# Kernel optimization log

Measured on AMD Instinct MI355X. Metric: run time of the kernel, lower is better.

## Reference

```python
import itertools
import jax, jax.numpy as jnp
import numpy as np
from jax import lax

INT_STEPS = 7
DOWN = 2


def _sample(vol, coords):
    """Trilinear sample vol [C, D, H, W] at voxel coords [3, D2, H2, W2].
    Matches torch grid_sample(align_corners=True, padding_mode='zeros') after
    voxelmorph's voxel->[-1,1] normalization (i.e. plain voxel coordinates)."""
    dims = vol.shape[1:]
    c0f = jnp.floor(coords)
    frac = coords - c0f
    c0 = c0f.astype(jnp.int32)
    out = jnp.zeros((vol.shape[0],) + coords.shape[1:], vol.dtype)
    for corner in itertools.product((0, 1), repeat=3):
        w = jnp.ones(coords.shape[1:], vol.dtype)
        valid = True
        idxs = []
        for ax in range(3):
            idx = c0[ax] + corner[ax]
            w = w * (frac[ax] if corner[ax] else 1.0 - frac[ax])
            valid = valid & (idx >= 0) & (idx < dims[ax])
            idxs.append(jnp.clip(idx, 0, dims[ax] - 1))
        out = out + vol[:, idxs[0], idxs[1], idxs[2]] * (w * valid)
    return out


def _grid(shape, dtype):
    return jnp.stack(jnp.meshgrid(*[jnp.arange(s, dtype=dtype) for s in shape], indexing='ij'))


def _warp(src, flow):
    # SpatialTransformer: sample src at identity grid + flow (voxel coords)
    return _sample(src, _grid(src.shape[1:], flow.dtype) + flow)


def _resize(x, out_shape):
    # F.interpolate trilinear, align_corners=True: src = i*(in-1)/(out-1)
    coords = jnp.stack(jnp.meshgrid(
        *[jnp.linspace(0.0, s_in - 1.0, s_out, dtype=x.dtype)
          for s_in, s_out in zip(x.shape[1:], out_shape)], indexing='ij'))
    return _sample(x, coords)


def _flow_single(pos_flow, label):
    # pos_flow: [3, D, H, W], label: [1, D, H, W]
    full = pos_flow.shape[1:]
    down_shape = tuple(s // DOWN for s in full)
    # ResizeTransform(int_downsize): factor=1/DOWN<1 -> resize then scale
    f = _resize(pos_flow, down_shape) * (1.0 / DOWN)
    # VecInt: scaling and squaring
    f = f * (1.0 / (2 ** INT_STEPS))
    for _ in range(INT_STEPS):
        f = f + _warp(f, f)
    # ResizeTransform(1/int_downsize): factor=DOWN>1 -> scale then resize
    f = _resize(f * float(DOWN), full)
    moved = _warp(label, f)
    return moved, f


def setup_inputs() -> dict:
    key = jax.random.key(0)
    k1, k2, k3 = jax.random.split(key, 3)
    B, F, D, H, W = 1, 16, 128, 128, 128
    features = jax.random.normal(k1, (B, F, D, H, W), jnp.float32)
    moving_label = jax.random.uniform(k2, (B, 1, D, H, W), jnp.float32)
    # conv weight initialized Normal(0, 1e-5), bias zeros (as in module)
    weight = jax.random.normal(k3, (3, F, 3, 3, 3), jnp.float32) * 1e-5
    bias = jnp.zeros((3,), jnp.float32)
    return {"features": features, "moving_label": moving_label,
            "weight": weight, "bias": bias}


def reference(features, moving_label, weight, bias):
    pos_flow = lax.conv_general_dilated(
        features, weight, window_strides=(1, 1, 1),
        padding=[(1, 1)] * 3,
        dimension_numbers=('NCDHW', 'OIDHW', 'NCDHW'))
    pos_flow = pos_flow + bias[None, :, None, None, None]
    moved, flow = jax.vmap(_flow_single)(pos_flow, moving_label)
    return moved, flow
```

## Files before the change

### kernel.cpp

```cpp
#include <hip/hip_runtime.h>


#define V128 2097152
#define V64  262144

typedef __attribute__((ext_vector_type(2))) float f32x2;
typedef float f32x2u __attribute__((ext_vector_type(2), aligned(4)));

template <int C>
__device__ __forceinline__ void trisample(const float* __restrict__ vol,
                                          int D, int H, int W, int cstride,
                                          float cz, float cy, float cx,
                                          float* out) {
    float fz = floorf(cz), fy = floorf(cy), fx = floorf(cx);
    int iz = (int)fz, iy = (int)fy, ix = (int)fx;
    float tz = cz - fz, ty = cy - fy, tx = cx - fx;
#pragma unroll
    for (int c = 0; c < C; ++c) out[c] = 0.0f;
#pragma unroll
    for (int dz = 0; dz < 2; ++dz) {
#pragma unroll
        for (int dy = 0; dy < 2; ++dy) {
#pragma unroll
            for (int dx = 0; dx < 2; ++dx) {
                int z = iz + dz, y = iy + dy, x = ix + dx;
                float w = (dz ? tz : 1.0f - tz) *
                          (dy ? ty : 1.0f - ty) *
                          (dx ? tx : 1.0f - tx);
                bool valid = (z >= 0) && (z < D) && (y >= 0) && (y < H) &&
                             (x >= 0) && (x < W);
                int zc = min(max(z, 0), D - 1);
                int yc = min(max(y, 0), H - 1);
                int xc = min(max(x, 0), W - 1);
                int base = (zc * H + yc) * W + xc;
                float wv = valid ? w : 0.0f;
#pragma unroll
                for (int c = 0; c < C; ++c)
                    out[c] += vol[c * cstride + base] * wv;
            }
        }
    }
}

template <int SI>
__device__ __forceinline__ void lds_lerp3(const float* __restrict__ f,
                                          float pz, float py, float px,
                                          float* out) {
    constexpr int NI = SI * SI * SI;
    float fz = floorf(pz), fy = floorf(py), fx = floorf(px);
    int iz = (int)fz, iy = (int)fy, ix = (int)fx;
    float tz = pz - fz, ty = py - fy, tx = px - fx;
    int b = (iz * SI + iy) * SI + ix;
    float wz0 = 1.0f - tz, wy0 = 1.0f - ty, wx0 = 1.0f - tx;
#pragma unroll
    for (int c = 0; c < 3; ++c) {
        const float* fc = f + c * NI;
        float v00 = fc[b] * wx0 + fc[b + 1] * tx;
        float v01 = fc[b + SI] * wx0 + fc[b + SI + 1] * tx;
        float v10 = fc[b + SI * SI] * wx0 + fc[b + SI * SI + 1] * tx;
        float v11 = fc[b + SI * SI + SI] * wx0 + fc[b + SI * SI + SI + 1] * tx;
        out[c] = wz0 * (wy0 * v00 + ty * v01) + tz * (wy0 * v10 + ty * v11);
    }
}

template <int SI, int NT>
__device__ __forceinline__ void step_lds(const float* __restrict__ in,
                                         float* __restrict__ out, int tid) {
    constexpr int SO = SI - 2;
    constexpr int NI = SI * SI * SI;
    constexpr int NO = SO * SO * SO;
    for (int i = tid; i < NO; i += NT) {
        int xx = i % SO, yy = (i / SO) % SO, zz = i / (SO * SO);
        int la = ((zz + 1) * SI + (yy + 1)) * SI + (xx + 1);
        float fz = in[la], fy = in[la + NI], fx = in[la + 2 * NI];
        float sm[3];
        lds_lerp3<SI>(in, (zz + 1) + fz, (yy + 1) + fy, (xx + 1) + fx, sm);
        out[i] = fz + sm[0];
        out[i + NO] = fy + sm[1];
        out[i + 2 * NO] = fx + sm[2];
    }
}

template <int NT>
__device__ __forceinline__ void step_to_global(const float* __restrict__ in,
                                               float* __restrict__ gout,
                                               int tx, int ty, int tz,
                                               int tid) {
    constexpr int SI = 10;
    constexpr int NI = SI * SI * SI;
    for (int i = tid; i < 512; i += NT) {
        int xx = i & 7, yy = (i >> 3) & 7, zz = i >> 6;
        int la = ((zz + 1) * SI + (yy + 1)) * SI + (xx + 1);
        float fz = in[la], fy = in[la + NI], fx = in[la + 2 * NI];
        float sm[3];
        lds_lerp3<SI>(in, (zz + 1) + fz, (yy + 1) + fy, (xx + 1) + fx, sm);
        int n3 = ((((tz + zz) << 12) + ((ty + yy) << 6) + (tx + xx))) * 3;
        gout[n3] = fz + sm[0];
        gout[n3 + 1] = fy + sm[1];
        gout[n3 + 2] = fx + sm[2];
    }
}

__global__ __launch_bounds__(256) void conv_kernel(
    const float* __restrict__ feat, const float* __restrict__ weight,
    const float* __restrict__ bias, float* __restrict__ pf) {
    __shared__ float smem[2][4356];
    const int tid = threadIdx.x;
    const int x0 = blockIdx.x * 64, y0 = blockIdx.y * 4, z0 = blockIdx.z * 8;
    const int lx = tid & 63, ly = tid >> 6;

    int goff[16];
    int laddr[16];
    unsigned vmask = 0;
#pragma unroll
    for (int k = 0; k < 16; ++k) {
        int s = tid + 256 * k;
        int col = s / 10;
        int zz = s - col * 10;
        int xx = col % 66;
        int yy = col / 66;
        laddr[k] = col * 11 + zz;
        bool intile = (k < 15) || (tid < 120);
        int gx = x0 + xx - 1, gy = y0 + yy - 1, gz = z0 + zz - 1;
        bool ok = intile && ((unsigned)gx < 128u) && ((unsigned)gy < 128u) &&
                  ((unsigned)gz < 128u);
        goff[k] = (gz << 14) + (gy << 7) + gx;
        if (ok) vmask |= (1u << k);
    }

    f32x2 acc[3][4];
#pragma unroll
    for (int o = 0; o < 3; ++o)
#pragma unroll
        for (int zp = 0; zp < 4; ++zp) acc[o][zp] = (f32x2)(0.0f);

    {
        float vals[16];
#pragma unroll
        for (int k = 0; k < 16; ++k) {
            vals[k] = 0.0f;
            if (vmask & (1u << k)) vals[k] = feat[goff[k]];
        }
#pragma unroll
        for (int k = 0; k < 16; ++k)
            if (k < 15 || tid < 120) smem[0][laddr[k]] = vals[k];
    }

    for (int c = 0; c < 16; ++c) {
        __syncthreads();
        if (c + 1 < 16) {
            const float* fc = feat + ((c + 1) << 21);
            float* buf = smem[(c + 1) & 1];
            float vals[16];
#pragma unroll
            for (int k = 0; k < 16; ++k) {
                vals[k] = 0.0f;
                if (vmask & (1u << k)) vals[k] = fc[goff[k]];
            }
#pragma unroll
            for (int k = 0; k < 16; ++k)
                if (k < 15 || tid < 120) buf[laddr[k]] = vals[k];
        }
        const float* buf = smem[c & 1];
        const float* wc = weight + c * 27;
#pragma unroll
        for (int dy = 0; dy < 3; ++dy) {
#pragma unroll
            for (int dx = 0; dx < 3; ++dx) {
                const float* p = buf + ((ly + dy) * 66 + lx + dx) * 11;
                f32x2 pv[5];
                f32x2 qv[4];
#pragma unroll
                for (int k2 = 0; k2 < 5; ++k2)
                    pv[k2] = *(const f32x2u*)(p + 2 * k2);
#pragma unroll
                for (int k2 = 0; k2 < 4; ++k2)
                    qv[k2] = *(const f32x2u*)(p + 2 * k2 + 1);
#pragma unroll
                for (int o = 0; o < 3; ++o) {
                    float w0 = wc[o * 432 + 0 + dy * 3 + dx];
                    float w1 = wc[o * 432 + 9 + dy * 3 + dx];
                    float w2 = wc[o * 432 + 18 + dy * 3 + dx];
#pragma unroll
                    for (int zp = 0; zp < 4; ++zp) {
                        acc[o][zp] += pv[zp] * (f32x2)(w0);
                        acc[o][zp] += qv[zp] * (f32x2)(w1);
                        acc[o][zp] += pv[zp + 1] * (f32x2)(w2);
                    }
                }
            }
        }
    }

    float b0 = bias[0], b1 = bias[1], b2 = bias[2];
#pragma unroll
    for (int zp = 0; zp < 4; ++zp) {
        int vox0 = ((z0 + 2 * zp) << 14) + ((y0 + ly) << 7) + x0 + lx;
#pragma unroll
        for (int h = 0; h < 2; ++h) {
            int m3 = (vox0 + (h << 14)) * 3;
            pf[m3] = (h ? acc[0][zp].y : acc[0][zp].x) + b0;
            pf[m3 + 1] = (h ? acc[1][zp].y : acc[1][zp].x) + b1;
            pf[m3 + 2] = (h ? acc[2][zp].y : acc[2][zp].x) + b2;
        }
    }
}

__global__ __launch_bounds__(512) void f2_kernel(
    const float* __restrict__ pf, float* __restrict__ gout) {
    __shared__ float A[3 * 2744];
    __shared__ float B[3 * 1728];
    const int tid = threadIdx.x;
    const int tx = blockIdx.x * 8, ty = blockIdx.y * 8, tz = blockIdx.z * 8;
    const int rbx = tx - 3, rby = ty - 3, rbz = tz - 3;
    const float s2 = 127.0f / 63.0f;
    const float k = 1.0f / 256.0f;
    for (int i = tid; i < 2744; i += 512) {
        int xx = i % 14, yy = (i / 14) % 14, zz = i / 196;
        int gz = rbz + zz, gy = rby + yy, gx = rbx + xx;
        float v0 = 0.0f, v1 = 0.0f, v2 = 0.0f;
        if ((unsigned)gz < 64u && (unsigned)gy < 64u && (unsigned)gx < 64u) {
            float cz = gz * s2, cy = gy * s2, cx = gx * s2;
            int iz = min((int)cz, 126);
            int iy = min((int)cy, 126);
            int ix = min((int)cx, 126);
            float tzf = cz - (float)iz;
            float tyf = cy - (float)iy;
            float txf = cx - (float)ix;
            float wz[2] = {1.0f - tzf, tzf};
            float wy[2] = {1.0f - tyf, tyf};
            float wx[2] = {1.0f - txf, txf};
            int b = ((iz << 14) + (iy << 7) + ix) * 3;
#pragma unroll
            for (int dz = 0; dz < 2; ++dz)
#pragma unroll
                for (int dy = 0; dy < 2; ++dy)
#pragma unroll
                    for (int dx = 0; dx < 2; ++dx) {
                        float w = wz[dz] * wy[dy] * wx[dx];
                        int bb = b + dz * (3 << 14) + dy * (3 << 7) + dx * 3;
                        v0 += pf[bb] * w;
                        v1 += pf[bb + 1] * w;
                        v2 += pf[bb + 2] * w;
                    }
        }
        A[i] = v0 * k;
        A[i + 2744] = v1 * k;
        A[i + 2 * 2744] = v2 * k;
    }
    __syncthreads();
    step_lds<14, 512>(A, B, tid);
    __syncthreads();
    step_lds<12, 512>(B, A, tid);
    __syncthreads();
    step_to_global<512>(A, gout, tx, ty, tz, tid);
}

__global__ __launch_bounds__(512) void f3_kernel(
    const float* __restrict__ gin, float* __restrict__ gout) {
    __shared__ float A[3 * 2744];
    __shared__ float B[3 * 1728];
    const int tid = threadIdx.x;
    const int tx = blockIdx.x * 8, ty = blockIdx.y * 8, tz = blockIdx.z * 8;
    const int rbx = tx - 3, rby = ty - 3, rbz = tz - 3;
    for (int i = tid; i < 2744; i += 512) {
        int xx = i % 14, yy = (i / 14) % 14, zz = i / 196;
        int gz = rbz + zz, gy = rby + yy, gx = rbx + xx;
        float v0 = 0.0f, v1 = 0.0f, v2 = 0.0f;
        if ((unsigned)gz < 64u && (unsigned)gy < 64u && (unsigned)gx < 64u) {
            int n3 = ((gz << 12) + (gy << 6) + gx) * 3;
            v0 = gin[n3];
            v1 = gin[n3 + 1];
            v2 = gin[n3 + 2];
        }
        A[i] = v0;
        A[i + 2744] = v1;
        A[i + 2 * 2744] = v2;
    }
    __syncthreads();
    step_lds<14, 512>(A, B, tid);
    __syncthreads();
    step_lds<12, 512>(B, A, tid);
    __syncthreads();
    step_to_global<512>(A, gout, tx, ty, tz, tid);
}

__global__ __launch_bounds__(512) void f4_kernel(
    const float* __restrict__ gin, const float* __restrict__ label,
    float* __restrict__ moved, float* __restrict__ flow) {
    __shared__ float A[3 * 2197];
    __shared__ float B[3 * 1331];
    const int tid = threadIdx.x;
    const int ttx = blockIdx.x, tty = blockIdx.y, ttz = blockIdx.z;
    const int r0x = (1008 * ttx) / 127 - 1;
    const int r0y = (1008 * tty) / 127 - 1;
    const int r0z = (1008 * ttz) / 127 - 1;
    const int rbx = r0x - 1, rby = r0y - 1, rbz = r0z - 1;
    for (int i = tid; i < 2197; i += 512) {
        int xx = i % 13, yy = (i / 13) % 13, zz = i / 169;
        int gz = rbz + zz, gy = rby + yy, gx = rbx + xx;
        float v0 = 0.0f, v1 = 0.0f, v2 = 0.0f;
        if ((unsigned)gz < 64u && (unsigned)gy < 64u && (unsigned)gx < 64u) {
            int n3 = ((gz << 12) + (gy << 6) + gx) * 3;
            v0 = gin[n3];
            v1 = gin[n3 + 1];
            v2 = gin[n3 + 2];
        }
        A[i] = v0;
        A[i + 2197] = v1;
        A[i + 2 * 2197] = v2;
    }
    __syncthreads();
    step_lds<13, 512>(A, B, tid);
    __syncthreads();
    const float s3 = 63.0f / 127.0f;
    for (int i = tid; i < 4096; i += 512) {
        int lx = i & 15, ly = (i >> 4) & 15, lz = i >> 8;
        int gx = ttx * 16 + lx, gy = tty * 16 + ly, gz = ttz * 16 + lz;
        float f[3];
        lds_lerp3<11>(B, gz * s3 - (float)r0z, gy * s3 - (float)r0y,
                      gx * s3 - (float)r0x, f);
        float fz = 2.0f * f[0], fy = 2.0f * f[1], fx = 2.0f * f[2];
        int m = (gz << 14) + (gy << 7) + gx;
        flow[m] = fz;
        flow[m + V128] = fy;
        flow[m + 2 * V128] = fx;
        float mv[1];
        trisample<1>(label, 128, 128, 128, 0, gz + fz, gy + fy, gx + fx, mv);
        moved[m] = mv[0];
    }
}

extern "C" void kernel_launch(void* const* d_in, const int* in_sizes, int n_in,
                              void* d_out, int out_size, void* d_ws,
                              size_t ws_size, hipStream_t stream) {
    const float* features = (const float*)d_in[0];
    const float* label = (const float*)d_in[1];
    const float* weight = (const float*)d_in[2];
    const float* bias = (const float*)d_in[3];
    float* out = (float*)d_out;
    float* moved = out;
    float* flow = out + V128;
    float* fA = (float*)d_ws;
    float* fB = fA + 3 * V64;

    conv_kernel<<<dim3(2, 32, 16), 256, 0, stream>>>(features, weight, bias,
                                                     flow);
    f2_kernel<<<dim3(8, 8, 8), 512, 0, stream>>>(flow, fA);
    f3_kernel<<<dim3(8, 8, 8), 512, 0, stream>>>(fA, fB);
    f4_kernel<<<dim3(8, 8, 8), 512, 0, stream>>>(fB, label, moved, flow);
}
```

Before: 325.3 us.

## Split downsample into separate kernel and reorder conv LDS load mapping

The downsample resize moves out of the first squaring kernel into a standalone per-voxel kernel that writes to the unused 'moved' output buffer. Both squaring stages then reuse one generic f23 kernel. Before, each block resampled its whole halo region, so overlapping halos were downsampled repeatedly; now every voxel is downsampled once. The cost is an extra launch and a round trip through global memory. Separately, the conv tile load now maps threads with x fastest instead of z fastest, so global reads coalesce better, though the LDS store pattern changes.

```diff
diff --git a/kernel.cpp b/kernel.cpp
--- a/kernel.cpp
+++ b/kernel.cpp
@@ -115,11 +115,11 @@
 #pragma unroll
     for (int k = 0; k < 16; ++k) {
         int s = tid + 256 * k;
-        int col = s / 10;
-        int zz = s - col * 10;
-        int xx = col % 66;
-        int yy = col / 66;
-        laddr[k] = col * 11 + zz;
+        int xx = s % 66;
+        int r = s / 66;
+        int yy = r % 6;
+        int zz = r / 6;
+        laddr[k] = (yy * 66 + xx) * 11 + zz;
         bool intile = (k < 15) || (tid < 120);
         int gx = x0 + xx - 1, gy = y0 + yy - 1, gz = z0 + zz - 1;
         bool ok = intile && ((unsigned)gx < 128u) && ((unsigned)gy < 128u) &&
@@ -206,57 +206,43 @@
     }
 }
 
-__global__ __launch_bounds__(512) void f2_kernel(
-    const float* __restrict__ pf, float* __restrict__ gout) {
-    __shared__ float A[3 * 2744];
-    __shared__ float B[3 * 1728];
-    const int tid = threadIdx.x;
-    const int tx = blockIdx.x * 8, ty = blockIdx.y * 8, tz = blockIdx.z * 8;
-    const int rbx = tx - 3, rby = ty - 3, rbz = tz - 3;
+__global__ __launch_bounds__(256) void ds_kernel(const float* __restrict__ pf,
+                                                 float* __restrict__ dsf) {
+    int i = blockIdx.x * 256 + threadIdx.x;
+    int gx = i & 63, gy = (i >> 6) & 63, gz = i >> 12;
     const float s2 = 127.0f / 63.0f;
     const float k = 1.0f / 256.0f;
-    for (int i = tid; i < 2744; i += 512) {
-        int xx = i % 14, yy = (i / 14) % 14, zz = i / 196;
-        int gz = rbz + zz, gy = rby + yy, gx = rbx + xx;
-        float v0 = 0.0f, v1 = 0.0f, v2 = 0.0f;
-        if ((unsigned)gz < 64u && (unsigned)gy < 64u && (unsigned)gx < 64u) {
-            float cz = gz * s2, cy = gy * s2, cx = gx * s2;
-            int iz = min((int)cz, 126);
-            int iy = min((int)cy, 126);
-            int ix = min((int)cx, 126);
-            float tzf = cz - (float)iz;
-            float tyf = cy - (float)iy;
-            float txf = cx - (float)ix;
-            float wz[2] = {1.0f - tzf, tzf};
-            float wy[2] = {1.0f - tyf, tyf};
-            float wx[2] = {1.0f - txf, txf};
-            int b = ((iz << 14) + (iy << 7) + ix) * 3;
-#pragma unroll
-            for (int dz = 0; dz < 2; ++dz)
-#pragma unroll
-                for (int dy = 0; dy < 2; ++dy)
-#pragma unroll
-                    for (int dx = 0; dx < 2; ++dx) {
-                        float w = wz[dz] * wy[dy] * wx[dx];
-                        int bb = b + dz * (3 << 14) + dy * (3 << 7) + dx * 3;
-                        v0 += pf[bb] * w;
-                        v1 += pf[bb + 1] * w;
-                        v2 += pf[bb + 2] * w;
-                    }
-        }
-        A[i] = v0 * k;
-        A[i + 2744] = v1 * k;
-        A[i + 2 * 2744] = v2 * k;
-    }
-    __syncthreads();
-    step_lds<14, 512>(A, B, tid);
-    __syncthreads();
-    step_lds<12, 512>(B, A, tid);
-    __syncthreads();
-    step_to_global<512>(A, gout, tx, ty, tz, tid);
-}
-
-__global__ __launch_bounds__(512) void f3_kernel(
+    float cz = gz * s2, cy = gy * s2, cx = gx * s2;
+    int iz = min((int)cz, 126);
+    int iy = min((int)cy, 126);
+    int ix = min((int)cx, 126);
+    float tzf = cz - (float)iz;
+    float tyf = cy - (float)iy;
+    float txf = cx - (float)ix;
+    float wz[2] = {1.0f - tzf, tzf};
+    float wy[2] = {1.0f - tyf, tyf};
+    float wx[2] = {1.0f - txf, txf};
+    int b = ((iz << 14) + (iy << 7) + ix) * 3;
+    float v0 = 0.0f, v1 = 0.0f, v2 = 0.0f;
+#pragma unroll
+    for (int dz = 0; dz < 2; ++dz)
+#pragma unroll
+        for (int dy = 0; dy < 2; ++dy)
+#pragma unroll
+            for (int dx = 0; dx < 2; ++dx) {
+                float w = wz[dz] * wy[dy] * wx[dx];
+                int bb = b + dz * (3 << 14) + dy * (3 << 7) + dx * 3;
+                v0 += pf[bb] * w;
+                v1 += pf[bb + 1] * w;
+                v2 += pf[bb + 2] * w;
+            }
+    int o3 = i * 3;
+    dsf[o3] = v0 * k;
+    dsf[o3 + 1] = v1 * k;
+    dsf[o3 + 2] = v2 * k;
+}
+
+__global__ __launch_bounds__(512) void f23_kernel(
     const float* __restrict__ gin, float* __restrict__ gout) {
     __shared__ float A[3 * 2744];
     __shared__ float B[3 * 1728];
@@ -341,12 +327,14 @@
     float* out = (float*)d_out;
     float* moved = out;
     float* flow = out + V128;
+    float* dsf = moved;
     float* fA = (float*)d_ws;
     float* fB = fA + 3 * V64;
 
     conv_kernel<<<dim3(2, 32, 16), 256, 0, stream>>>(features, weight, bias,
                                                      flow);
-    f2_kernel<<<dim3(8, 8, 8), 512, 0, stream>>>(flow, fA);
-    f3_kernel<<<dim3(8, 8, 8), 512, 0, stream>>>(fA, fB);
+    ds_kernel<<<dim3(1024), 256, 0, stream>>>(flow, dsf);
+    f23_kernel<<<dim3(8, 8, 8), 512, 0, stream>>>(dsf, fA);
+    f23_kernel<<<dim3(8, 8, 8), 512, 0, stream>>>(fA, fB);
     f4_kernel<<<dim3(8, 8, 8), 512, 0, stream>>>(fB, label, moved, flow);
 }
```

After: 292.5 us. 10.1% less time.
